# Kernel tuning notes

Hardware: AMD Instinct MI355X
Metric: run time of the kernel (lower is better)

## Reference

```python
import jax, jax.numpy as jnp
import numpy as np

LIMIT = 20      # module's self.limit: only first 20 unique labels per mask participate
EPS = 1e-5      # BatchNorm2d default eps


def _ccl(mask):
    """4-connected component labeling via max-label propagation.
    mask: [H, W] bool. Returns int32 labels, 0 = background; each component's
    label is (1 + max flat pixel index) inside it, so jnp.sort order matches
    torch.unique's ascending order up to a component permutation."""
    H, W = mask.shape
    init = jnp.where(mask, jnp.arange(1, H * W + 1, dtype=jnp.int32).reshape(H, W), 0)

    def prop(l):
        up = jnp.pad(l[1:, :], ((0, 1), (0, 0)))
        dn = jnp.pad(l[:-1, :], ((1, 0), (0, 0)))
        lf = jnp.pad(l[:, 1:], ((0, 0), (0, 1)))
        rt = jnp.pad(l[:, :-1], ((0, 0), (1, 0)))
        m = jnp.maximum(jnp.maximum(l, up), jnp.maximum(dn, jnp.maximum(lf, rt)))
        return jnp.where(mask, m, 0)

    def cond(st):
        return ~st[1]

    def body(st):
        l, _ = st
        nl = prop(l)
        return nl, jnp.all(nl == l)

    labels, _ = jax.lax.while_loop(cond, body, (init, jnp.array(False)))
    return labels


def _region_stats(xb, labels):
    """Compact-rank the LIMIT smallest unique labels (rank 0 = background 0)
    and compute per-component means of xb over pixels.
    xb: [C, H, W]; labels: [H, W] int32.
    Returns means [LIMIT, C], has [LIMIT] bool, seg [P] (LIMIT = dump)."""
    P = labels.size
    lab = labels.reshape(P)
    order = jnp.argsort(lab)
    s = lab[order]
    isnew = jnp.concatenate([jnp.ones((1,), bool), s[1:] != s[:-1]])
    rank_sorted = (jnp.cumsum(isnew) - 1).astype(jnp.int32)  # ascending-unique rank
    rank = jnp.zeros((P,), jnp.int32).at[order].set(rank_sorted)
    valid = (rank < LIMIT) & (lab > 0)   # rank 0 is background label 0
    seg = jnp.where(valid, rank, LIMIT)
    C = xb.shape[0]
    xf = xb.reshape(C, P).T              # [P, C]
    sums = jax.ops.segment_sum(xf, seg, num_segments=LIMIT + 1)[:LIMIT]
    cnts = jax.ops.segment_sum(jnp.ones((P,), xb.dtype), seg, num_segments=LIMIT + 1)[:LIMIT]
    means = sums / jnp.maximum(cnts, 1.0)[:, None]
    has = cnts > 0
    return means, has, seg


def _forward(x, conv_w, conv_b, gamma, beta):
    # attn conv (3x3, SAME) + Softmax2d (softmax over channels)
    logits = jax.lax.conv_general_dilated(
        x, conv_w, (1, 1), 'SAME', dimension_numbers=('NCHW', 'OIHW', 'NCHW')
    ) + conv_b[None, :, None, None]
    out_attn = jax.nn.softmax(logits, axis=1)
    am = jnp.argmax(out_attn, axis=1)            # [B, H, W]
    lab1 = jax.vmap(_ccl)(am == 1)
    lab2 = jax.vmap(_ccl)(am == 2)

    def per_batch(xb, l1, l2):
        m1, h1, s1 = _region_stats(xb, l1)       # means indexed by uniq rank (rank0=bg)
        m2, h2, s2 = _region_stats(xb, l2)
        M = m1 @ m2.T                             # M[i, j] = mean_i . mean_j, mm[i-1, j-1] in torch
        pf = jnp.where(h1[:, None] & h2[None, :], 1.0 + M, 1.0)
        # Each valid (i, j) pair multiplies area1(i) and area2(j) by (1 + mm);
        # sequential in-place updates compound into these closed-form products.
        mult1 = jnp.prod(pf, axis=1)              # [LIMIT]
        mult2 = jnp.prod(pf, axis=0)
        f1 = jnp.where(s1 < LIMIT, mult1[jnp.clip(s1, 0, LIMIT - 1)], 1.0)
        f2 = jnp.where(s2 < LIMIT, mult2[jnp.clip(s2, 0, LIMIT - 1)], 1.0)
        return (f1 * f2).reshape(l1.shape)

    factor = jax.vmap(per_batch)(x, lab1, lab2)  # [B, H, W]
    x2 = x * factor[:, None, :, :]
    # BatchNorm2d in training mode (batch stats, biased var)
    mean = x2.mean(axis=(0, 2, 3))
    var = x2.var(axis=(0, 2, 3))
    xn = (x2 - mean[None, :, None, None]) * jax.lax.rsqrt(var + EPS)[None, :, None, None]
    xn = xn * gamma[None, :, None, None] + beta[None, :, None, None]
    return xn, out_attn


def setup_inputs() -> dict:
    key = jax.random.key(0)
    k1, k2 = jax.random.split(key)
    B, C, H, W = 8, 256, 160, 160
    x = jax.random.normal(k1, (B, C, H, W), dtype=jnp.float32)
    conv_w = jax.random.normal(k2, (3, C, 3, 3), dtype=jnp.float32) * 0.05
    conv_b = jnp.zeros((3,), jnp.float32)
    gamma = jnp.ones((C,), jnp.float32)
    beta = jnp.zeros((C,), jnp.float32)
    return {'x': x, 'conv_w': conv_w, 'conv_b': conv_b, 'gamma': gamma, 'beta': beta}


def reference(x, conv_w, conv_b, gamma, beta):
    return _forward(x, conv_w, conv_b, gamma, beta)
```

## Files before the change

### kernel.cpp

```cpp
#include <hip/hip_runtime.h>
#include <stdint.h>
#include <float.h>

#define HW 160
#define PP 25600
#define BB 8
#define CCH 256
#define NIMG 16
#define LIM 20
#define MAXC 12800
#define CPG 32
#define NCG (CCH/CPG)
#define ROWS 8
#define RT (HW/ROWS)

typedef unsigned char u8;
typedef unsigned long long u64;

__global__ void kzero(float* binsA, float* binsB, int* cnts, int* ncomp,
                      double* sumA, double* sumB, int* lcnt){
  int i = blockIdx.x*256 + threadIdx.x;
  if(i < BB*40*CCH){ binsA[i]=0.f; binsB[i]=0.f; }
  if(i < BB*40) cnts[i]=0;
  if(i < NIMG) ncomp[i]=0;
  if(i < CCH){ sumA[i]=0.0; sumB[i]=0.0; }
  if(i < BB) lcnt[i]=0;
}

__device__ __forceinline__ void gload16(const float* g, float* l){
  __builtin_amdgcn_global_load_lds((const __attribute__((address_space(1))) void*)g,
                                   (__attribute__((address_space(3))) void*)l, 16, 0, 0);
}

__global__ __launch_bounds__(256) void kconv(const float* __restrict__ x,
                                             const float* __restrict__ w,
                                             float* __restrict__ partial,
                                             double* __restrict__ sumA,
                                             double* __restrict__ sumB){
  const int b = blockIdx.z, cg = blockIdx.y, bx = blockIdx.x, r0 = bx*ROWS;
  const int tid = threadIdx.x;
  __shared__ float wl[CPG][28];
  __shared__ float xt[2][1600];
  __shared__ float bsA[CPG][4], bsB[CPG][4];
  for(int t=tid; t<CPG*27; t+=256){
    int cc=t/27, k=t%27;
    wl[cc][k] = w[((k/9)*CCH + cg*CPG + cc)*9 + (k%9)];
  }
  for(int i=tid; i<2*1600; i+=256) ((float*)xt)[i]=0.f;
  if(tid<CPG*4){ ((float*)bsA)[tid]=0.f; ((float*)bsB)[tid]=0.f; }

  int src_row = r0 - 1, ldsoff = 0, nchunks = 400;
  if(bx == 0){ src_row = 0; ldsoff = 160; nchunks = 360; }
  if(bx == RT-1){ nchunks = 360; }
  const float* xg = x + ((size_t)b*CCH + cg*CPG)*PP;
  const int wid = tid>>6, lane = tid&63;
  const int ch0 = wid*64 + lane, ch1 = 256 + wid*64 + lane;

  #define STAGE(bsel, cc_) { \
    const float* gsrc = xg + (size_t)(cc_)*PP + src_row*HW; \
    if(ch0 < nchunks) gload16(gsrc + ch0*4, &xt[bsel][ldsoff + wid*256]); \
    if(ch1 < nchunks) gload16(gsrc + ch1*4, &xt[bsel][ldsoff + 1024 + wid*256]); }

  const int or_ = tid>>5, j0 = (tid&31)*5;

  __syncthreads();
  STAGE(0, 0);
  __syncthreads();

  float acc[3][5];
  #pragma unroll
  for(int o=0;o<3;o++)
    #pragma unroll
    for(int px=0;px<5;px++) acc[o][px]=0.f;

  int cur=0;
  for(int cc=0; cc<CPG; cc++){
    if(cc+1<CPG) STAGE(cur^1, cc+1);
    float sv[3][7];
    #pragma unroll
    for(int rr=0;rr<3;rr++){
      const float* row = &xt[cur][(or_+rr)*HW];
      sv[rr][0] = (j0>0) ? row[j0-1] : 0.f;
      #pragma unroll
      for(int k=1;k<6;k++) sv[rr][k] = row[j0-1+k];
      sv[rr][6] = (j0+5<HW) ? row[j0+5] : 0.f;
    }
    float s=0.f, s2=0.f;
    #pragma unroll
    for(int k=1;k<6;k++){ float vv=sv[1][k]; s+=vv; s2=fmaf(vv,vv,s2); }
    #pragma unroll
    for(int off=32; off; off>>=1){ s += __shfl_xor(s,off); s2 += __shfl_xor(s2,off); }
    if(lane==0){ bsA[cc][wid] += s; bsB[cc][wid] += s2; }
    #pragma unroll
    for(int o=0;o<3;o++){
      #pragma unroll
      for(int kr=0;kr<3;kr++){
        float w0 = wl[cc][o*9+kr*3+0];
        float w1 = wl[cc][o*9+kr*3+1];
        float w2 = wl[cc][o*9+kr*3+2];
        #pragma unroll
        for(int px=0;px<5;px++)
          acc[o][px] = fmaf(w0, sv[kr][px], fmaf(w1, sv[kr][px+1], fmaf(w2, sv[kr][px+2], acc[o][px])));
      }
    }
    __syncthreads();
    cur ^= 1;
  }
  #undef STAGE

  if(tid < CPG){
    float a = bsA[tid][0]+bsA[tid][1]+bsA[tid][2]+bsA[tid][3];
    float bq = bsB[tid][0]+bsB[tid][1]+bsB[tid][2]+bsB[tid][3];
    atomicAdd(&sumA[cg*CPG+tid], (double)a);
    atomicAdd(&sumB[cg*CPG+tid], (double)bq);
  }
  size_t base = ((size_t)(cg*BB+b)*3)*PP + (size_t)(r0+or_)*HW + j0;
  #pragma unroll
  for(int o=0;o<3;o++){
    #pragma unroll
    for(int px=0;px<5;px++) partial[base + (size_t)o*PP + px] = acc[o][px];
  }
}

__global__ void ksoftmax(const float* __restrict__ partial, const float* __restrict__ cb,
                         float* __restrict__ attn, u8* __restrict__ am,
                         int* __restrict__ parent, int* __restrict__ maxidx){
  int idx = blockIdx.x*256 + threadIdx.x;
  if(idx >= BB*PP) return;
  int b = idx/PP, p = idx%PP;
  float l[3];
  #pragma unroll
  for(int o=0;o<3;o++){
    float s = cb[o];
    #pragma unroll
    for(int cg=0;cg<NCG;cg++) s += partial[(((size_t)cg*BB+b)*3+o)*PP + p];
    l[o]=s;
  }
  int a=0; float best=l[0];
  if(l[1]>best){best=l[1];a=1;}
  if(l[2]>best){best=l[2];a=2;}
  float e0=__expf(l[0]-best);
  float e1=__expf(l[1]-best);
  float e2=__expf(l[2]-best);
  float inv = 1.f/(e0+e1+e2);
  attn[((size_t)b*3+0)*PP+p]=e0*inv;
  attn[((size_t)b*3+1)*PP+p]=e1*inv;
  attn[((size_t)b*3+2)*PP+p]=e2*inv;
  am[idx]=(u8)a;
  int i1 = (b*2+0)*PP + p, i2 = (b*2+1)*PP + p;
  parent[i1] = (a==1) ? p : -1;
  parent[i2] = (a==2) ? p : -1;
  maxidx[i1] = -1;
  maxidx[i2] = -1;
}

__device__ inline int froot(int* par, int x){
  while(true){
    int p = par[x];
    if(p == x) return x;
    int g = par[p];
    if(g == p) return p;
    par[x] = g;
    x = g;
  }
}
__device__ inline void unite(int* par, int a, int b){
  int ra = froot(par,a), rb = froot(par,b);
  while(ra != rb){
    if(ra > rb){ int t=ra; ra=rb; rb=t; }
    int old = atomicCAS(&par[rb], rb, ra);
    if(old == rb) return;
    rb = froot(par, old);
    ra = froot(par, ra);
  }
}
__global__ void kunion(int* parent){
  int idx = blockIdx.x*256 + threadIdx.x;
  if(idx >= NIMG*PP) return;
  int img = idx/PP, p = idx%PP;
  int* par = parent + img*PP;
  if(par[p] < 0) return;
  int i = p/HW, j = p%HW;
  if(j < HW-1 && par[p+1] >= 0) unite(par, p, p+1);
  if(i < HW-1 && par[p+HW] >= 0) unite(par, p, p+HW);
}
__global__ void kflatmax(int* parent, int* __restrict__ maxidx){
  int idx = blockIdx.x*256 + threadIdx.x;
  if(idx >= NIMG*PP) return;
  int img = idx/PP, p = idx%PP;
  int* par = parent + img*PP;
  if(par[p] < 0) return;
  int r = froot(par, p);
  par[p] = r;
  atomicMax(&maxidx[img*PP + r], p);
}

__global__ void kcompact(const int* __restrict__ parent, const int* __restrict__ maxidx,
                         int* __restrict__ rootlist, int* __restrict__ ncomp){
  int idx = blockIdx.x*256 + threadIdx.x;
  int img = idx/PP, p = idx%PP;
  bool isroot = (parent[idx] == p);
  u64 mask = __ballot(isroot);
  int lane = threadIdx.x & 63;
  int wid = threadIdx.x >> 6;
  __shared__ int wcnt[4];
  __shared__ int bbase;
  if(lane == 0) wcnt[wid] = __popcll(mask);
  __syncthreads();
  if(threadIdx.x == 0){
    int tot = wcnt[0]+wcnt[1]+wcnt[2]+wcnt[3];
    bbase = (tot>0) ? atomicAdd(&ncomp[img], tot) : 0;
  }
  __syncthreads();
  if(isroot){
    int mybase = bbase;
    for(int wv=0; wv<wid; wv++) mybase += wcnt[wv];
    mybase += __popcll(mask & ((lane==63)? ~0ull>>1 : ((1ull<<lane)-1)));
    rootlist[img*MAXC + mybase] = (maxidx[idx]<<16) | p;
  }
}

__global__ __launch_bounds__(256) void kselect(const int* __restrict__ rootlist, const int* __restrict__ ncomp,
                        const int* __restrict__ parent,
                        int* __restrict__ selr, int* __restrict__ nsel){
  int img = blockIdx.x, t = threadIdx.x;
  __shared__ int sv[256];
  __shared__ int scnt[256];
  const int* par = parent + img*PP;
  int cnt=0;
  for(int p=t; p<PP; p+=256) cnt += (par[p]>=0) ? 1 : 0;
  scnt[t]=cnt; __syncthreads();
  for(int off=128; off; off>>=1){ if(t<off) scnt[t]+=scnt[t+off]; __syncthreads(); }
  int K = LIM - ((scnt[0] < PP) ? 1 : 0);
  int nr = ncomp[img];
  const int* rl = rootlist + img*MAXC;
  int prev = -1, n = 0;
  for(int k=0;k<K;k++){
    int best = 0x7fffffff;
    for(int q=t; q<nr; q+=256){ int v=rl[q]; if(v>prev && v<best) best=v; }
    sv[t]=best; __syncthreads();
    for(int off=128; off; off>>=1){
      if(t<off && sv[t+off]<sv[t]) sv[t]=sv[t+off];
      __syncthreads();
    }
    int bv = sv[0]; __syncthreads();
    if(bv == 0x7fffffff) break;
    if(t==0) selr[img*LIM+k] = bv & 0xffff;
    prev = bv; n = k+1;
  }
  if(t==0) nsel[img] = n;
}

__global__ void kseg(const u8* __restrict__ am, const int* __restrict__ parent,
                     const int* __restrict__ selr, const int* __restrict__ nsel,
                     u8* __restrict__ seg, int* __restrict__ cnts,
                     int* __restrict__ list, int* __restrict__ lcnt){
  int idx = blockIdx.x*256 + threadIdx.x;
  __shared__ int cl[40];
  if(threadIdx.x < 40) cl[threadIdx.x] = 0;
  __syncthreads();
  int b = idx/PP, p = idx%PP;
  int a = am[idx];
  int code = 40;
  if(a > 0){
    int img = b*2 + a - 1;
    int r = parent[img*PP + p];
    int n = nsel[img];
    for(int k=0;k<n;k++){
      if(selr[img*LIM + k] == r){ code = (a-1)*LIM + k; break; }
    }
  }
  seg[idx] = (u8)code;
  if(code < 40){
    atomicAdd(&cl[code], 1);
    int pos = atomicAdd(&lcnt[b], 1);
    list[b*PP + pos] = (code<<16) | p;
  }
  __syncthreads();
  if(threadIdx.x < 40 && cl[threadIdx.x] > 0) atomicAdd(&cnts[b*40 + threadIdx.x], cl[threadIdx.x]);
}

__global__ __launch_bounds__(256) void kbins2(const float* __restrict__ x, const int* __restrict__ list,
                                              const int* __restrict__ lcnt,
                                              float* __restrict__ binsA, float* __restrict__ binsB){
  const int b = blockIdx.y;
  const int n = lcnt[b];
  const int c = threadIdx.x;
  for(int e = blockIdx.x; e < n; e += gridDim.x){
    int ent = list[b*PP + e];
    int p = ent & 0xffff;
    int code = ent >> 16;
    float v = x[((size_t)b*CCH + c)*PP + p];
    atomicAdd(&binsA[((size_t)b*40 + code)*CCH + c], v);
    atomicAdd(&binsB[((size_t)b*40 + code)*CCH + c], v*v);
  }
}

__global__ __launch_bounds__(256) void kmult(const float* __restrict__ binsA, const int* __restrict__ cnts,
                       const int* __restrict__ nsel, double* __restrict__ multd,
                       float* __restrict__ multf){
  const int b = blockIdx.x, t = threadIdx.x;
  __shared__ float m1[LIM][CCH+1], m2[LIM][CCH+1];
  __shared__ float Ml[LIM*LIM];
  const int n1 = nsel[b*2+0], n2 = nsel[b*2+1];
  for(int k=0;k<LIM;k++){
    m1[k][t] = (k<n1) ? binsA[((size_t)b*40 + k)*CCH + t] / (float)cnts[b*40 + k] : 0.f;
    m2[k][t] = (k<n2) ? binsA[((size_t)b*40 + LIM + k)*CCH + t] / (float)cnts[b*40 + LIM + k] : 0.f;
  }
  __syncthreads();
  for(int pid=t; pid<LIM*LIM; pid+=256){
    int i = pid/LIM, j = pid%LIM;
    float d = 0.f;
    for(int c=0;c<CCH;c++) d += m1[i][c]*m2[j][c];
    Ml[pid] = 1.f + d;
  }
  __syncthreads();
  if(t < LIM){
    double pr=1.0;
    for(int j=0;j<LIM;j++) pr *= (double)Ml[t*LIM+j];
    multd[b*40 + t] = pr;
    multf[b*40 + t] = (float)pr;
  } else if(t>=64 && t<64+LIM){
    int j=t-64; double pr=1.0;
    for(int i=0;i<LIM;i++) pr *= (double)Ml[i*LIM+j];
    multd[b*40 + LIM + j] = pr;
    multf[b*40 + LIM + j] = (float)pr;
  }
}

__global__ void kscale(const float* __restrict__ binsA, const float* __restrict__ binsB,
                       const double* __restrict__ sumA, const double* __restrict__ sumB,
                       const double* __restrict__ multd, const float* __restrict__ gamma,
                       const float* __restrict__ beta, float* __restrict__ scale, float* __restrict__ shift){
  int c = threadIdx.x;
  double s = sumA[c], s2 = sumB[c];
  for(int b=0;b<BB;b++){
    for(int sc=0; sc<40; sc++){
      double f = multd[b*40+sc];
      s  += (f-1.0)   * (double)binsA[((size_t)b*40+sc)*CCH + c];
      s2 += (f*f-1.0) * (double)binsB[((size_t)b*40+sc)*CCH + c];
    }
  }
  const double N = (double)BB*PP;
  double mean = s/N;
  double devsq = s2 - N*mean*mean;
  bool ovf = !(devsq <= 3.3e38) || !(fabs(s) <= 3.3e38) || !(s2 < 1e300);
  if(ovf){
    scale[c] = 0.f;
    shift[c] = beta[c];
  } else {
    double var = devsq/N;
    double inv = 1.0 / sqrt(var + 1e-5);
    float scv = (float)inv * gamma[c];
    scale[c] = scv;
    shift[c] = beta[c] - (float)mean * scv;
  }
}

__global__ __launch_bounds__(256) void kout(const float* __restrict__ x, const u8* __restrict__ seg,
                      const float* __restrict__ multf, const float* __restrict__ scale,
                      const float* __restrict__ shift, float* __restrict__ out){
  size_t idx = ((size_t)blockIdx.x*256 + threadIdx.x)*4;
  int b = (int)(idx / ((size_t)CCH*PP));
  int c = (int)((idx / PP) % CCH);
  int p = (int)(idx % PP);
  __shared__ float fm[41];
  if(threadIdx.x <= 40) fm[threadIdx.x] = (threadIdx.x<40) ? multf[b*40 + threadIdx.x] : 1.f;
  __syncthreads();
  float sc = scale[c], sh = shift[c];
  float4 o;
  if(sc == 0.f){
    o.x = sh; o.y = sh; o.z = sh; o.w = sh;
  } else {
    float4 xv = *(const float4*)(x + idx);
    uchar4 sv = *(const uchar4*)(seg + (size_t)b*PP + p);
    o.x = xv.x * fm[sv.x] * sc + sh;
    o.y = xv.y * fm[sv.y] * sc + sh;
    o.z = xv.z * fm[sv.z] * sc + sh;
    o.w = xv.w * fm[sv.w] * sc + sh;
  }
  *(float4*)(out + idx) = o;
}

extern "C" void kernel_launch(void* const* d_in, const int* in_sizes, int n_in,
                              void* d_out, int out_size, void* d_ws, size_t ws_size,
                              hipStream_t stream){
  (void)in_sizes; (void)n_in; (void)out_size; (void)ws_size;
  const float* x  = (const float*)d_in[0];
  const float* w  = (const float*)d_in[1];
  const float* cb = (const float*)d_in[2];
  const float* gamma = (const float*)d_in[3];
  const float* beta  = (const float*)d_in[4];
  float* out  = (float*)d_out;
  float* attn = out + (size_t)BB*CCH*PP;

  float* partial  = out;
  int*   parent   = (int*)(out + 20000000);
  int*   maxidx   = (int*)(out + 20500000);
  u8*    am       = (u8*)(out + 21000000);
  float* binsA    = out + 21100000;
  float* binsB    = out + 21200000;
  int*   rootlist = (int*)(out + 21300000);
  int*   ncomp    = (int*)(out + 21600000);
  int*   list     = (int*)(out + 21700000);
  int*   lcnt     = (int*)(out + 22000000);
  double* sumA    = (double*)(out + 22100000);
  double* sumB    = (double*)(out + 22101000);

  double* multd = (double*)d_ws;
  float* multf  = (float*)((char*)d_ws + 2560);
  float* scale  = multf + BB*40;
  float* shift  = scale + CCH;
  int* selr     = (int*)(shift + CCH);
  int* nsel     = selr + NIMG*LIM;
  int* cnts     = nsel + NIMG;
  u8* seg       = (u8*)(cnts + BB*40);

  kzero<<<dim3(320), dim3(256), 0, stream>>>(binsA, binsB, cnts, ncomp, sumA, sumB, lcnt);
  kconv<<<dim3(RT,NCG,BB), dim3(256), 0, stream>>>(x, w, partial, sumA, sumB);
  ksoftmax<<<dim3(800), dim3(256), 0, stream>>>(partial, cb, attn, am, parent, maxidx);
  kunion<<<dim3(1600), dim3(256), 0, stream>>>(parent);
  kflatmax<<<dim3(1600), dim3(256), 0, stream>>>(parent, maxidx);
  kcompact<<<dim3(1600), dim3(256), 0, stream>>>(parent, maxidx, rootlist, ncomp);
  kselect<<<dim3(NIMG), dim3(256), 0, stream>>>(rootlist, ncomp, parent, selr, nsel);
  kseg<<<dim3(800), dim3(256), 0, stream>>>(am, parent, selr, nsel, seg, cnts, list, lcnt);
  kbins2<<<dim3(64,BB), dim3(256), 0, stream>>>(x, list, lcnt, binsA, binsB);
  kmult<<<dim3(BB), dim3(256), 0, stream>>>(binsA, cnts, nsel, multd, multf);
  kscale<<<dim3(1), dim3(256), 0, stream>>>(binsA, binsB, sumA, sumB, multd, gamma, beta, scale, shift);
  kout<<<dim3(51200), dim3(256), 0, stream>>>(x, seg, multf, scale, shift, out);
}
```

Before: 269.9 us.

## Fuse connected-component labeling pipeline into one LDS-resident kernel per mask image

```diff
diff --git a/kernel.cpp b/kernel.cpp
--- a/kernel.cpp
+++ b/kernel.cpp
@@ -8,21 +8,20 @@
 #define CCH 256
 #define NIMG 16
 #define LIM 20
-#define MAXC 12800
 #define CPG 32
 #define NCG (CCH/CPG)
 #define ROWS 8
 #define RT (HW/ROWS)
+#define NPT 25
 
 typedef unsigned char u8;
 typedef unsigned long long u64;
 
-__global__ void kzero(float* binsA, float* binsB, int* cnts, int* ncomp,
+__global__ void kzero(float* binsA, float* binsB, int* cnts,
                       double* sumA, double* sumB, int* lcnt){
   int i = blockIdx.x*256 + threadIdx.x;
   if(i < BB*40*CCH){ binsA[i]=0.f; binsB[i]=0.f; }
   if(i < BB*40) cnts[i]=0;
-  if(i < NIMG) ncomp[i]=0;
   if(i < CCH){ sumA[i]=0.0; sumB[i]=0.0; }
   if(i < BB) lcnt[i]=0;
 }
@@ -123,8 +122,7 @@
 }
 
 __global__ void ksoftmax(const float* __restrict__ partial, const float* __restrict__ cb,
-                         float* __restrict__ attn, u8* __restrict__ am,
-                         int* __restrict__ parent, int* __restrict__ maxidx){
+                         float* __restrict__ attn, u8* __restrict__ am){
   int idx = blockIdx.x*256 + threadIdx.x;
   if(idx >= BB*PP) return;
   int b = idx/PP, p = idx%PP;
@@ -147,11 +145,6 @@
   attn[((size_t)b*3+1)*PP+p]=e1*inv;
   attn[((size_t)b*3+2)*PP+p]=e2*inv;
   am[idx]=(u8)a;
-  int i1 = (b*2+0)*PP + p, i2 = (b*2+1)*PP + p;
-  parent[i1] = (a==1) ? p : -1;
-  parent[i2] = (a==2) ? p : -1;
-  maxidx[i1] = -1;
-  maxidx[i2] = -1;
 }
 
 __device__ inline int froot(int* par, int x){
@@ -174,110 +167,117 @@
     ra = froot(par, ra);
   }
 }
-__global__ void kunion(int* parent){
-  int idx = blockIdx.x*256 + threadIdx.x;
-  if(idx >= NIMG*PP) return;
-  int img = idx/PP, p = idx%PP;
-  int* par = parent + img*PP;
-  if(par[p] < 0) return;
-  int i = p/HW, j = p%HW;
-  if(j < HW-1 && par[p+1] >= 0) unite(par, p, p+1);
-  if(i < HW-1 && par[p+HW] >= 0) unite(par, p, p+HW);
-}
-__global__ void kflatmax(int* parent, int* __restrict__ maxidx){
-  int idx = blockIdx.x*256 + threadIdx.x;
-  if(idx >= NIMG*PP) return;
-  int img = idx/PP, p = idx%PP;
-  int* par = parent + img*PP;
-  if(par[p] < 0) return;
-  int r = froot(par, p);
-  par[p] = r;
-  atomicMax(&maxidx[img*PP + r], p);
-}
-
-__global__ void kcompact(const int* __restrict__ parent, const int* __restrict__ maxidx,
-                         int* __restrict__ rootlist, int* __restrict__ ncomp){
-  int idx = blockIdx.x*256 + threadIdx.x;
-  int img = idx/PP, p = idx%PP;
-  bool isroot = (parent[idx] == p);
-  u64 mask = __ballot(isroot);
-  int lane = threadIdx.x & 63;
-  int wid = threadIdx.x >> 6;
-  __shared__ int wcnt[4];
-  __shared__ int bbase;
-  if(lane == 0) wcnt[wid] = __popcll(mask);
-  __syncthreads();
-  if(threadIdx.x == 0){
-    int tot = wcnt[0]+wcnt[1]+wcnt[2]+wcnt[3];
-    bbase = (tot>0) ? atomicAdd(&ncomp[img], tot) : 0;
-  }
-  __syncthreads();
-  if(isroot){
-    int mybase = bbase;
-    for(int wv=0; wv<wid; wv++) mybase += wcnt[wv];
-    mybase += __popcll(mask & ((lane==63)? ~0ull>>1 : ((1ull<<lane)-1)));
-    rootlist[img*MAXC + mybase] = (maxidx[idx]<<16) | p;
-  }
-}
-
-__global__ __launch_bounds__(256) void kselect(const int* __restrict__ rootlist, const int* __restrict__ ncomp,
-                        const int* __restrict__ parent,
-                        int* __restrict__ selr, int* __restrict__ nsel){
-  int img = blockIdx.x, t = threadIdx.x;
-  __shared__ int sv[256];
-  __shared__ int scnt[256];
-  const int* par = parent + img*PP;
-  int cnt=0;
-  for(int p=t; p<PP; p+=256) cnt += (par[p]>=0) ? 1 : 0;
-  scnt[t]=cnt; __syncthreads();
-  for(int off=128; off; off>>=1){ if(t<off) scnt[t]+=scnt[t+off]; __syncthreads(); }
-  int K = LIM - ((scnt[0] < PP) ? 1 : 0);
-  int nr = ncomp[img];
-  const int* rl = rootlist + img*MAXC;
+
+__global__ __launch_bounds__(1024) void kccl(const u8* __restrict__ am,
+                                             u8* __restrict__ seg, int* __restrict__ cnts,
+                                             int* __restrict__ list, int* __restrict__ lcnt,
+                                             int* __restrict__ nsel){
+  __shared__ int par[PP];
+  __shared__ int rootkeys[PP/2];
+  __shared__ int redbuf[16];
+  __shared__ int selr_s[LIM];
+  __shared__ int cntl[LIM];
+  __shared__ int nrk, bigcnt, bval;
+  const int img = blockIdx.x, b = img>>1, m = (img&1)+1;
+  const int tid = threadIdx.x, lane = tid&63, wv = tid>>6;
+  const u8* amb = am + b*PP;
+
+  if(tid==0) nrk = 0;
+  if(tid<LIM) cntl[tid] = 0;
+  int mcnt = 0;
+  #pragma unroll
+  for(int i=0;i<NPT;i++){
+    int p = tid + i*1024;
+    bool in = (amb[p]==m);
+    par[p] = in ? p : -1;
+    mcnt += in;
+  }
+  #pragma unroll
+  for(int off=32; off; off>>=1) mcnt += __shfl_xor(mcnt, off);
+  if(lane==0) redbuf[wv] = mcnt;
+  __syncthreads();
+  if(tid==0){ int s=0; for(int i=0;i<16;i++) s+=redbuf[i]; bigcnt=s; }
+  __syncthreads();
+  const int K = LIM - (bigcnt < PP ? 1 : 0);
+  #pragma unroll
+  for(int i=0;i<NPT;i++){
+    int p = tid + i*1024;
+    if(par[p] < 0) continue;
+    int j = p % HW;
+    if(j < HW-1 && par[p+1] >= 0) unite(par, p, p+1);
+    if(p+HW < PP && par[p+HW] >= 0) unite(par, p, p+HW);
+  }
+  __syncthreads();
+  int rloc[NPT];
+  #pragma unroll
+  for(int i=0;i<NPT;i++){
+    int p = tid + i*1024;
+    int v = par[p];
+    if(v < 0){ rloc[i] = -1; continue; }
+    int r = froot(par, p);
+    par[p] = r;
+    rloc[i] = r;
+  }
+  __syncthreads();
+  #pragma unroll
+  for(int i=0;i<NPT;i++){
+    int p = tid + i*1024;
+    if(rloc[i] >= 0) atomicMax(&par[rloc[i]], p);
+  }
+  __syncthreads();
+  #pragma unroll
+  for(int i=0;i<NPT;i++){
+    int p = tid + i*1024;
+    int v = par[p];
+    if(v >= p && v >= 0){
+      int pos = atomicAdd(&nrk, 1);
+      rootkeys[pos] = (v<<16) | p;
+    }
+  }
+  __syncthreads();
+  const int nr = nrk;
   int prev = -1, n = 0;
   for(int k=0;k<K;k++){
     int best = 0x7fffffff;
-    for(int q=t; q<nr; q+=256){ int v=rl[q]; if(v>prev && v<best) best=v; }
-    sv[t]=best; __syncthreads();
-    for(int off=128; off; off>>=1){
-      if(t<off && sv[t+off]<sv[t]) sv[t]=sv[t+off];
-      __syncthreads();
-    }
-    int bv = sv[0]; __syncthreads();
+    for(int q=tid; q<nr; q+=1024){
+      int v = rootkeys[q];
+      if(v > prev && v < best) best = v;
+    }
+    #pragma unroll
+    for(int off=32; off; off>>=1){ int o = __shfl_xor(best, off); if(o < best) best = o; }
+    if(lane==0) redbuf[wv] = best;
+    __syncthreads();
+    if(tid==0){ int s=redbuf[0]; for(int i=1;i<16;i++) if(redbuf[i]<s) s=redbuf[i]; bval=s; }
+    __syncthreads();
+    int bv = bval;
     if(bv == 0x7fffffff) break;
-    if(t==0) selr[img*LIM+k] = bv & 0xffff;
+    if(tid==0) selr_s[n] = bv & 0xffff;
     prev = bv; n = k+1;
   }
-  if(t==0) nsel[img] = n;
-}
-
-__global__ void kseg(const u8* __restrict__ am, const int* __restrict__ parent,
-                     const int* __restrict__ selr, const int* __restrict__ nsel,
-                     u8* __restrict__ seg, int* __restrict__ cnts,
-                     int* __restrict__ list, int* __restrict__ lcnt){
-  int idx = blockIdx.x*256 + threadIdx.x;
-  __shared__ int cl[40];
-  if(threadIdx.x < 40) cl[threadIdx.x] = 0;
-  __syncthreads();
-  int b = idx/PP, p = idx%PP;
-  int a = am[idx];
-  int code = 40;
-  if(a > 0){
-    int img = b*2 + a - 1;
-    int r = parent[img*PP + p];
-    int n = nsel[img];
-    for(int k=0;k<n;k++){
-      if(selr[img*LIM + k] == r){ code = (a-1)*LIM + k; break; }
-    }
-  }
-  seg[idx] = (u8)code;
-  if(code < 40){
-    atomicAdd(&cl[code], 1);
-    int pos = atomicAdd(&lcnt[b], 1);
-    list[b*PP + pos] = (code<<16) | p;
-  }
-  __syncthreads();
-  if(threadIdx.x < 40 && cl[threadIdx.x] > 0) atomicAdd(&cnts[b*40 + threadIdx.x], cl[threadIdx.x]);
+  __syncthreads();
+  #pragma unroll
+  for(int i=0;i<NPT;i++){
+    int p = tid + i*1024;
+    int a = amb[p];
+    if(m==1 && a==0){ seg[b*PP+p] = 40; continue; }
+    if(a != m) continue;
+    int v = par[p];
+    int r = (v >= p) ? p : v;
+    int code = LIM;
+    for(int k=0;k<n;k++) if(selr_s[k]==r){ code=k; break; }
+    if(code < LIM){
+      atomicAdd(&cntl[code], 1);
+      int gc = (m-1)*LIM + code;
+      int pos = atomicAdd(&lcnt[b], 1);
+      list[b*PP + pos] = (gc<<16) | p;
+      seg[b*PP+p] = (u8)gc;
+    } else {
+      seg[b*PP+p] = 40;
+    }
+  }
+  __syncthreads();
+  if(tid < n) cnts[b*40 + (m-1)*LIM + tid] = cntl[tid];
+  if(tid==0) nsel[img] = n;
 }
 
 __global__ __launch_bounds__(256) void kbins2(const float* __restrict__ x, const int* __restrict__ list,
@@ -395,13 +395,9 @@
   float* attn = out + (size_t)BB*CCH*PP;
 
   float* partial  = out;
-  int*   parent   = (int*)(out + 20000000);
-  int*   maxidx   = (int*)(out + 20500000);
   u8*    am       = (u8*)(out + 21000000);
   float* binsA    = out + 21100000;
   float* binsB    = out + 21200000;
-  int*   rootlist = (int*)(out + 21300000);
-  int*   ncomp    = (int*)(out + 21600000);
   int*   list     = (int*)(out + 21700000);
   int*   lcnt     = (int*)(out + 22000000);
   double* sumA    = (double*)(out + 22100000);
@@ -411,19 +407,14 @@
   float* multf  = (float*)((char*)d_ws + 2560);
   float* scale  = multf + BB*40;
   float* shift  = scale + CCH;
-  int* selr     = (int*)(shift + CCH);
-  int* nsel     = selr + NIMG*LIM;
+  int* nsel     = (int*)(shift + CCH);
   int* cnts     = nsel + NIMG;
   u8* seg       = (u8*)(cnts + BB*40);
 
-  kzero<<<dim3(320), dim3(256), 0, stream>>>(binsA, binsB, cnts, ncomp, sumA, sumB, lcnt);
+  kzero<<<dim3(320), dim3(256), 0, stream>>>(binsA, binsB, cnts, sumA, sumB, lcnt);
   kconv<<<dim3(RT,NCG,BB), dim3(256), 0, stream>>>(x, w, partial, sumA, sumB);
-  ksoftmax<<<dim3(800), dim3(256), 0, stream>>>(partial, cb, attn, am, parent, maxidx);
-  kunion<<<dim3(1600), dim3(256), 0, stream>>>(parent);
-  kflatmax<<<dim3(1600), dim3(256), 0, stream>>>(parent, maxidx);
-  kcompact<<<dim3(1600), dim3(256), 0, stream>>>(parent, maxidx, rootlist, ncomp);
-  kselect<<<dim3(NIMG), dim3(256), 0, stream>>>(rootlist, ncomp, parent, selr, nsel);
-  kseg<<<dim3(800), dim3(256), 0, stream>>>(am, parent, selr, nsel, seg, cnts, list, lcnt);
+  ksoftmax<<<dim3(800), dim3(256), 0, stream>>>(partial, cb, attn, am);
+  kccl<<<dim3(NIMG), dim3(1024), 0, stream>>>(am, seg, cnts, list, lcnt, nsel);
   kbins2<<<dim3(64,BB), dim3(256), 0, stream>>>(x, list, lcnt, binsA, binsB);
   kmult<<<dim3(BB), dim3(256), 0, stream>>>(binsA, cnts, nsel, multd, multf);
   kscale<<<dim3(1), dim3(256), 0, stream>>>(binsA, binsB, sumA, sumB, multd, gamma, beta, scale, shift);
```

New measurement: 301.0 us. 11.5% more time.
